# Kernel tuning notes

Hardware: AMD Instinct MI355X
Metric: run time of the kernel (lower is better)

Reference implementation:

```python
import jax, jax.numpy as jnp
import numpy as np

N_HEADS = 16
EPS = 1e-4


def setup_inputs() -> dict:
    key = jax.random.key(0)
    ks = jax.random.split(key, 9)
    B, L, E = 4, 4096, 1024
    s = 1.0 / np.sqrt(E)
    return {
        "x": jax.random.normal(ks[0], (B, L, E), dtype=jnp.float32),
        "Wq": jax.random.normal(ks[1], (E, E), dtype=jnp.float32) * s,
        "bq": jax.random.normal(ks[2], (E,), dtype=jnp.float32) * 0.01,
        "Wk": jax.random.normal(ks[3], (E, E), dtype=jnp.float32) * s,
        "bk": jax.random.normal(ks[4], (E,), dtype=jnp.float32) * 0.01,
        "Wv": jax.random.normal(ks[5], (E, E), dtype=jnp.float32) * s,
        "bv": jax.random.normal(ks[6], (E,), dtype=jnp.float32) * 0.01,
        "Wo": jax.random.normal(ks[7], (E, E), dtype=jnp.float32) * s,
        "bo": jax.random.normal(ks[8], (E,), dtype=jnp.float32) * 0.01,
    }


def _cosformer(x, Wq, bq, Wk, bk, Wv, bv, Wo, bo):
    B, L, E = x.shape
    H = N_HEADS
    hd = E // H
    # torch Linear: y = x @ W.T + b; self-attention so q=k=v source is x
    q = jax.nn.relu(jnp.einsum('ble,fe->blf', x, Wq) + bq)
    k = jax.nn.relu(jnp.einsum('ble,fe->blf', x, Wk) + bk)
    v = jnp.einsum('ble,fe->blf', x, Wv) + bv
    # (B, L, E) -> (B*H, L, hd)  [matches torch view(L, B*H, hd).transpose(0,1)]
    def split_heads(t):
        return t.reshape(B, L, H, hd).transpose(0, 2, 1, 3).reshape(B * H, L, hd)
    q, k, v = split_heads(q), split_heads(k), split_heads(v)
    m = L  # src_len == tgt_len
    idx = (np.pi / 2) * jnp.arange(1, m + 1, dtype=jnp.float32) / m  # (m,)
    sin = jnp.sin(idx)[None, :, None]
    cos = jnp.cos(idx)[None, :, None]
    q_ = jnp.concatenate([q * sin, q * cos], axis=-1)  # (BH, L, 2hd)
    k_ = jnp.concatenate([k * sin, k * cos], axis=-1)
    kv = jnp.einsum('nld,nlm->ndm', k_, v)             # (BH, 2hd, hd)
    z = 1.0 / jnp.maximum(jnp.einsum('nld,nd->nl', q_, k_.sum(axis=1)), EPS)
    attn = jnp.einsum('nld,ndm->nlm', q_, kv) * z[:, :, None]  # (BH, L, hd)
    # (B*H, L, hd) -> (B, L, E)
    out = attn.reshape(B, H, L, hd).transpose(0, 2, 1, 3).reshape(B, L, E)
    return jnp.einsum('ble,fe->blf', out, Wo) + bo


def reference(x, Wq, bq, Wk, bk, Wv, bv, Wo, bo):
    return _cosformer(x, Wq, bq, Wk, bk, Wv, bv, Wo, bo)
```

## Files before the change

kernel.cpp:

```cpp
#include <hip/hip_runtime.h>


typedef unsigned short u16;
typedef unsigned int u32;
typedef __attribute__((ext_vector_type(8))) __bf16 bf16x8;
typedef __attribute__((ext_vector_type(4))) float f32x4;

#define PI_HALF 1.57079632679489662f
#define EPS_Z 1e-4f

__device__ __forceinline__ u16 f32_to_bf16(float f) {
    union { float f; unsigned int u; } x; x.f = f;
    unsigned int lsb = (x.u >> 16) & 1u;
    x.u += 0x7fffu + lsb;
    return (u16)(x.u >> 16);
}

typedef __attribute__((address_space(1))) void amdgpu_global_t;
typedef __attribute__((address_space(3))) void amdgpu_lds_t;
__device__ __forceinline__ void async_load16(const u16* g, u16* l) {
    __builtin_amdgcn_global_load_lds((amdgpu_global_t*)g, (amdgpu_lds_t*)l, 16, 0, 0);
}

__global__ __launch_bounds__(256) void cvt_all(const float* __restrict__ x,
                                               const float* __restrict__ w0,
                                               const float* __restrict__ w1,
                                               const float* __restrict__ w2,
                                               const float* __restrict__ w3,
                                               u16* __restrict__ xb,
                                               u16* __restrict__ wcat) {
    const int bid = blockIdx.x;
    const float* src;
    u16* dst;
    int i;
    if (bid < 16384) {
        src = x; dst = xb;
        i = bid * 256 + threadIdx.x;
    } else {
        const int wb = bid - 16384;
        const int wsel = wb >> 10;
        src = (wsel == 0) ? w0 : (wsel == 1) ? w1 : (wsel == 2) ? w2 : w3;
        dst = wcat + (size_t)wsel * 1048576;
        i = (wb & 1023) * 256 + threadIdx.x;
    }
    float4 f = ((const float4*)src)[i];
    ushort4 o;
    o.x = f32_to_bf16(f.x); o.y = f32_to_bf16(f.y);
    o.z = f32_to_bf16(f.z); o.w = f32_to_bf16(f.w);
    ((ushort4*)dst)[i] = o;
}

__device__ __forceinline__ void gemm256_core(const u16* __restrict__ Abase,
                                             const u16* __restrict__ Bbase,
                                             u16* As, u16* Bs,
                                             f32x4 (&acc)[8][4]) {
    const int tid  = threadIdx.x;
    const int wave = tid >> 6;
    const int lane = tid & 63;
    const int quad = lane >> 4;
    const int l15  = lane & 15;
    const int wr   = wave >> 2;
    const int wc   = wave & 3;
    const int srow = tid >> 3;
    const int scg  = (tid & 7) ^ (srow & 7);

    const u16* Ag = Abase + ((long)srow << 10) + scg * 8;
    const u16* Bg = Bbase + ((long)srow << 10) + scg * 8;

    auto stage = [&](const u16* g, u16* lb, int hs, int t) {
        async_load16(g + ((long)hs << 16) + (t << 6), lb + hs * 4096);
    };
    auto rdA = [&](const u16* buf, int mf, int kk) -> bf16x8 {
        const int R = wr * 128 + mf * 16 + l15;
        return *(const bf16x8*)(buf + R * 64 + ((kk * 32 + quad * 8) ^ ((R & 7) * 8)));
    };
    auto rdB = [&](const u16* buf, int nf, int kk) -> bf16x8 {
        const int R = wc * 64 + nf * 16 + l15;
        return *(const bf16x8*)(buf + R * 64 + ((kk * 32 + quad * 8) ^ ((R & 7) * 8)));
    };

    bf16x8 a[4][2], b[4][2];
    auto mfma8 = [&](int i0, int j0) {
        __builtin_amdgcn_s_setprio(1);
#pragma unroll
        for (int i = 0; i < 4; ++i)
#pragma unroll
            for (int j = 0; j < 2; ++j)
#pragma unroll
                for (int kk = 0; kk < 2; ++kk)
                    acc[i0 + i][j0 + j] = __builtin_amdgcn_mfma_f32_16x16x32_bf16(
                        a[i][kk], b[j0 + j][kk], acc[i0 + i][j0 + j], 0, 0, 0);
        __builtin_amdgcn_s_setprio(0);
    };

#pragma unroll
    for (int hs = 0; hs < 4; ++hs) stage(Ag, As + wave * 512, hs, 0);
#pragma unroll
    for (int hs = 0; hs < 4; ++hs) stage(Bg, Bs + wave * 512, hs, 0);
#pragma unroll
    for (int hs = 0; hs < 4; ++hs) stage(Ag, As + 16384 + wave * 512, hs, 1);
#pragma unroll
    for (int hs = 0; hs < 4; ++hs) stage(Bg, Bs + 16384 + wave * 512, hs, 1);
    asm volatile("s_waitcnt vmcnt(8)" ::: "memory");
    __builtin_amdgcn_s_barrier();

#pragma unroll 1
    for (int t = 0; t < 16; ++t) {
        const int cur = t & 1;
        const u16* Ab = As + cur * 16384;
        const u16* Bb = Bs + cur * 16384;
        u16* lA = As + cur * 16384 + wave * 512;
        u16* lB = Bs + cur * 16384 + wave * 512;
        const bool pf = (t < 14);

#pragma unroll
        for (int i = 0; i < 4; ++i) { a[i][0] = rdA(Ab, i, 0); a[i][1] = rdA(Ab, i, 1); }
#pragma unroll
        for (int j = 0; j < 2; ++j) { b[j][0] = rdB(Bb, j, 0); b[j][1] = rdB(Bb, j, 1); }
        mfma8(0, 0);
#pragma unroll
        for (int j = 2; j < 4; ++j) { b[j][0] = rdB(Bb, j, 0); b[j][1] = rdB(Bb, j, 1); }
        mfma8(0, 2);
#pragma unroll
        for (int i = 0; i < 4; ++i) { a[i][0] = rdA(Ab, i + 4, 0); a[i][1] = rdA(Ab, i + 4, 1); }
        mfma8(4, 0);

        __builtin_amdgcn_s_barrier();
        asm volatile("" ::: "memory");
        if (pf) {
#pragma unroll
            for (int hs = 0; hs < 4; ++hs) stage(Bg, lB, hs, t + 2);
#pragma unroll
            for (int hs = 0; hs < 4; ++hs) stage(Ag, lA, hs, t + 2);
        }
        mfma8(4, 2);
        if (pf) {
            asm volatile("s_waitcnt vmcnt(8)" ::: "memory");
        } else {
            asm volatile("s_waitcnt vmcnt(0)" ::: "memory");
        }
        __builtin_amdgcn_s_barrier();
        asm volatile("" ::: "memory");
    }
}

__global__ __launch_bounds__(512, 2) void gemm_qkv(const u16* __restrict__ A,
                                                   const u16* __restrict__ Wcat,
                                                   const float* __restrict__ bq,
                                                   const float* __restrict__ bk,
                                                   const float* __restrict__ bv,
                                                   u16* __restrict__ qo,
                                                   u16* __restrict__ ko,
                                                   u16* __restrict__ vo) {
    __shared__ __align__(16) u16 As[32768];
    __shared__ __align__(16) u16 Bs[32768];
    const int bid = blockIdx.x;
    const int swz = (bid & 7) * 96 + (bid >> 3);
    const int bx  = swz / 12;
    const int byy = swz - bx * 12;
    const long tileM = (long)bx * 256;

    f32x4 acc[8][4] = {};
    gemm256_core(A + (tileM << 10), Wcat + ((long)byy << 18), As, Bs, acc);

    const int tid  = (int)threadIdx.x;
    const int wave = tid >> 6;
    const int lane = tid & 63;
    const int quad = lane >> 4, l15 = lane & 15;
    const int wr = wave >> 2, wc = wave & 3;
    const int mat = byy >> 2;
    const float* bias = (mat == 0) ? bq : (mat == 1) ? bk : bv;
    u16* outp = (mat == 0) ? qo : (mat == 1) ? ko : vo;
    const bool relu = (mat < 2);
    const int ncol0 = (byy & 3) * 256;

    const int rloc = tid >> 5;
    const int c8   = (tid & 31) * 8;
#pragma unroll 1
    for (int pass = 0; pass < 2; ++pass) {
        __syncthreads();
        if (wr == pass) {
#pragma unroll
            for (int i = 0; i < 8; ++i)
#pragma unroll
                for (int j = 0; j < 4; ++j) {
                    const int col = wc * 64 + j * 16 + l15;
                    const float bb = bias[ncol0 + col];
#pragma unroll
                    for (int r = 0; r < 4; ++r) {
                        const int row = i * 16 + quad * 4 + r;
                        float v = acc[i][j][r] + bb;
                        if (relu) v = fmaxf(v, 0.0f);
                        As[row * 256 + col] = f32_to_bf16(v);
                    }
                }
        }
        __syncthreads();
        const long gr0 = tileM + pass * 128;
#pragma unroll
        for (int it = 0; it < 8; ++it) {
            const int row = it * 16 + rloc;
            uint4 t4 = *(const uint4*)&As[row * 256 + c8];
            *(uint4*)&outp[(gr0 + row) * 1024 + ncol0 + c8] = t4;
        }
    }
}

__global__ __launch_bounds__(512, 2) void gemm_o(const u16* __restrict__ A,
                                                 const u16* __restrict__ Bw,
                                                 const float* __restrict__ bias,
                                                 float* __restrict__ Cout) {
    __shared__ __align__(16) u16 As[32768];
    __shared__ __align__(16) u16 Bs[32768];
    const int bid = blockIdx.x;
    const int swz = (bid & 7) * 32 + (bid >> 3);
    const long tileM = (long)(swz >> 2) * 256;
    const long tileN = (long)(swz & 3) * 256;

    f32x4 acc[8][4] = {};
    gemm256_core(A + (tileM << 10), Bw + (tileN << 10), As, Bs, acc);

    const int wave = (int)threadIdx.x >> 6;
    const int lane = (int)threadIdx.x & 63;
    const int quad = lane >> 4, l15 = lane & 15;
    const int wr = wave >> 2, wc = wave & 3;
#pragma unroll
    for (int j = 0; j < 4; ++j) {
        const long n = tileN + wc * 64 + j * 16 + l15;
        const float bb = bias[n];
#pragma unroll
        for (int i = 0; i < 8; ++i) {
            const long m0 = tileM + wr * 128 + i * 16 + quad * 4;
#pragma unroll
            for (int r = 0; r < 4; ++r)
                Cout[(m0 + r) * 1024 + n] = acc[i][j][r] + bb;
        }
    }
}

__global__ __launch_bounds__(256) void kv_mfma(const u16* __restrict__ kmat,
                                               const u16* __restrict__ vmat,
                                               float* __restrict__ part) {
    __shared__ u16 Ak[64 * 72];
    __shared__ u16 Bv[64 * 72];
    const int tid = threadIdx.x;
    const int wave = tid >> 6, lane = tid & 63;
    const int quad = lane >> 4, l15 = lane & 15;
    const int head = blockIdx.y;
    const int b = head >> 4, h = head & 15;
    const int l0 = blockIdx.x * 512;
    const int sl = tid >> 3;
    const int sc8 = tid & 7;
    const int scol = sl ^ ((sc8 & 3) << 3);
    const int krow_base = (wave & 1) * 32;
    const bool use_cos = (wave >> 1) != 0;
    const int mbase = wave * 32;

    float sv[8], cv[8], s2[8], c2[8];
#pragma unroll
    for (int e = 0; e < 8; e++) {
        float ang = (PI_HALF / 4096.0f) * (float)(l0 + quad * 8 + e + 1);
        sv[e] = sinf(ang); cv[e] = cosf(ang);
        float ang2 = ang + (PI_HALF / 4096.0f) * 32.0f;
        s2[e] = sinf(ang2); c2[e] = cosf(ang2);
    }
    const float cD = 0.99969881869620422f;
    const float sD = 0.02454122852291229f;

    bf16x8 onesf;
#pragma unroll
    for (int e = 0; e < 8; e++)
        onesf[e] = (l15 == 0) ? (__bf16)1.0f : (__bf16)0.0f;

    f32x4 acc[2][5] = {};

    long row = ((long)b * 4096 + l0 + sl) * 1024 + h * 64 + sc8 * 8;
    uint4 kkA = *(const uint4*)(kmat + row);
    uint4 vvA = *(const uint4*)(vmat + row);
    uint4 kkB = *(const uint4*)(kmat + row + 32 * 1024);
    uint4 vvB = *(const uint4*)(vmat + row + 32 * 1024);

#pragma unroll 1
    for (int kt = 0; kt < 8; kt++) {
        uint4 kkA_n = {}, vvA_n = {}, kkB_n = {}, vvB_n = {};
        if (kt < 7) {
            row += 64 * 1024;
            kkA_n = *(const uint4*)(kmat + row);
            vvA_n = *(const uint4*)(vmat + row);
            kkB_n = *(const uint4*)(kmat + row + 32 * 1024);
            vvB_n = *(const uint4*)(vmat + row + 32 * 1024);
        }
        {
            const u16* kp = (const u16*)&kkA;
            const u16* vp = (const u16*)&vvA;
            const u16* kp2 = (const u16*)&kkB;
            const u16* vp2 = (const u16*)&vvB;
#pragma unroll
            for (int e = 0; e < 8; e++) {
                const int d = sc8 * 8 + e;
                Ak[d * 72 + scol]      = kp[e];
                Bv[d * 72 + scol]      = vp[e];
                Ak[d * 72 + scol + 32] = kp2[e];
                Bv[d * 72 + scol + 32] = vp2[e];
            }
        }
        __syncthreads();

        bf16x8 af[2][2];
#pragma unroll
        for (int i = 0; i < 2; i++) {
            const int d = krow_base + i * 16 + l15;
            const int q2 = (quad ^ ((d >> 3) & 3)) * 8;
#pragma unroll
            for (int kk = 0; kk < 2; kk++) {
                bf16x8 raw = *(const bf16x8*)&Ak[d * 72 + kk * 32 + q2];
                bf16x8 sc;
#pragma unroll
                for (int e = 0; e < 8; e++) {
                    const float s = use_cos ? (kk ? c2[e] : cv[e])
                                            : (kk ? s2[e] : sv[e]);
                    sc[e] = (__bf16)((float)raw[e] * s);
                }
                af[i][kk] = sc;
            }
        }
        bf16x8 bfr[5][2];
#pragma unroll
        for (int j = 0; j < 4; j++) {
            const int n = j * 16 + l15;
            const int q2 = (quad ^ ((n >> 3) & 3)) * 8;
            bfr[j][0] = *(const bf16x8*)&Bv[n * 72 + q2];
            bfr[j][1] = *(const bf16x8*)&Bv[n * 72 + 32 + q2];
        }
        bfr[4][0] = onesf; bfr[4][1] = onesf;
#pragma unroll
        for (int i = 0; i < 2; i++)
#pragma unroll
            for (int j = 0; j < 5; j++) {
                acc[i][j] = __builtin_amdgcn_mfma_f32_16x16x32_bf16(
                    af[i][0], bfr[j][0], acc[i][j], 0, 0, 0);
                acc[i][j] = __builtin_amdgcn_mfma_f32_16x16x32_bf16(
                    af[i][1], bfr[j][1], acc[i][j], 0, 0, 0);
            }

#pragma unroll
        for (int e = 0; e < 8; e++) {
            float ns = sv[e] * cD + cv[e] * sD;
            cv[e] = cv[e] * cD - sv[e] * sD;
            sv[e] = ns;
            ns = s2[e] * cD + c2[e] * sD;
            c2[e] = c2[e] * cD - s2[e] * sD;
            s2[e] = ns;
        }
        __syncthreads();
        kkA = kkA_n; vvA = vvA_n; kkB = kkB_n; vvB = vvB_n;
    }

    float* op = part + ((long)blockIdx.x * 64 + head) * 10240;
#pragma unroll
    for (int i = 0; i < 2; i++)
#pragma unroll
        for (int j = 0; j < 5; j++)
#pragma unroll
            for (int r = 0; r < 4; r++)
                op[(mbase + i * 16 + quad * 4 + r) * 80 + j * 16 + l15] = acc[i][j][r];
}

__global__ __launch_bounds__(256) void kv_reduce_t(const float* __restrict__ part,
                                                   u16* __restrict__ Bt) {
    __shared__ float accs[32 * 81];
    const int head = blockIdx.y, d2t = blockIdx.x;
    const float* bp = part + (long)head * 10240 + d2t * 32 * 80;
    for (int idx = threadIdx.x; idx < 2560; idx += 256) {
        float s = 0.0f;
#pragma unroll
        for (int c = 0; c < 8; c++) s += bp[(long)c * 655360 + idx];
        const int d2 = idx / 80, n = idx - d2 * 80;
        accs[d2 * 81 + n] = s;
    }
    __syncthreads();
    for (int idx = threadIdx.x; idx < 2560; idx += 256) {
        const int n = idx >> 5, d2 = idx & 31;
        Bt[(long)head * 10240 + n * 128 + d2t * 32 + d2] = f32_to_bf16(accs[d2 * 81 + n]);
    }
}

__global__ __launch_bounds__(256) void attn_mfma(const u16* __restrict__ qb,
                                                 const u16* __restrict__ Bt,
                                                 u16* __restrict__ merged) {
    __shared__ __align__(16) u16 As[128 * 72];
    __shared__ __align__(16) u16 Bs[80 * 136];
    const int tid = threadIdx.x;
    const int wave = tid >> 6, lane = tid & 63;
    const int quad = lane >> 4, l15 = lane & 15;
    const int head = blockIdx.y;
    const int b = head >> 4, h = head & 15;
    const int tm0 = blockIdx.x * 256;
    const long b4 = (long)b * 4096;
    const int wm = wave * 32;

    for (int c = tid; c < 1280; c += 256) {
        const int row = c >> 4, c16 = c & 15;
        uint4 t = *(const uint4*)(Bt + (long)head * 10240 + row * 128 + c16 * 8);
        *(uint4*)&Bs[row * 136 + c16 * 8] = t;
    }

#pragma unroll 1
    for (int half = 0; half < 2; ++half) {
        const int tm = tm0 + half * 128;
        __syncthreads();
        for (int c = tid; c < 1024; c += 256) {
            const int row = c >> 3, c8 = c & 7;
            uint4 t = *(const uint4*)(qb + (b4 + tm + row) * 1024 + h * 64 + c8 * 8);
            *(uint4*)&As[row * 72 + c8 * 8] = t;
        }
        float snl[2], csl[2];
#pragma unroll
        for (int i = 0; i < 2; i++) {
            const int l = tm + wm + i * 16 + l15;
            const float idx = PI_HALF * (float)(l + 1) * (1.0f / 4096.0f);
            snl[i] = sinf(idx); csl[i] = cosf(idx);
        }
        __syncthreads();

        f32x4 acc[2][5] = {};
#pragma unroll
        for (int kb = 0; kb < 4; kb++) {
            const int qc = (kb & 1) * 32 + quad * 8;
            bf16x8 af[2];
#pragma unroll
            for (int i = 0; i < 2; i++) {
                bf16x8 raw = *(const bf16x8*)&As[(wm + i * 16 + l15) * 72 + qc];
                const float s = (kb < 2) ? snl[i] : csl[i];
                bf16x8 sc;
#pragma unroll
                for (int e = 0; e < 8; e++) sc[e] = (__bf16)((float)raw[e] * s);
                af[i] = sc;
            }
            bf16x8 bf[5];
#pragma unroll
            for (int j = 0; j < 5; j++)
                bf[j] = *(const bf16x8*)&Bs[(j * 16 + l15) * 136 + kb * 32 + quad * 8];
#pragma unroll
            for (int i = 0; i < 2; i++)
#pragma unroll
                for (int j = 0; j < 5; j++)
                    acc[i][j] = __builtin_amdgcn_mfma_f32_16x16x32_bf16(
                        af[i], bf[j], acc[i][j], 0, 0, 0);
        }

        __syncthreads();
#pragma unroll
        for (int i = 0; i < 2; i++) {
            float z[4];
#pragma unroll
            for (int r = 0; r < 4; r++) {
                const float den = __shfl(acc[i][4][r], lane & 0x30, 64);
                z[r] = 1.0f / fmaxf(den, EPS_Z);
            }
#pragma unroll
            for (int j = 0; j < 4; j++)
#pragma unroll
                for (int r = 0; r < 4; r++) {
                    const int row = wm + i * 16 + quad * 4 + r;
                    As[row * 64 + j * 16 + l15] = f32_to_bf16(acc[i][j][r] * z[r]);
                }
        }
        __syncthreads();
        const int rloc = tid >> 3, c8o = (tid & 7) * 8;
#pragma unroll
        for (int it = 0; it < 4; ++it) {
            const int row = it * 32 + rloc;
            uint4 t4 = *(const uint4*)&As[row * 64 + c8o];
            *(uint4*)&merged[(b4 + tm + row) * 1024 + h * 64 + c8o] = t4;
        }
    }
}

extern "C" void kernel_launch(void* const* d_in, const int* in_sizes, int n_in,
                              void* d_out, int out_size, void* d_ws, size_t ws_size,
                              hipStream_t stream) {
    (void)in_sizes; (void)n_in; (void)out_size; (void)ws_size;
    const float* x  = (const float*)d_in[0];
    const float* Wq = (const float*)d_in[1];
    const float* bq = (const float*)d_in[2];
    const float* Wk = (const float*)d_in[3];
    const float* bk = (const float*)d_in[4];
    const float* Wv = (const float*)d_in[5];
    const float* bv = (const float*)d_in[6];
    const float* Wo = (const float*)d_in[7];
    const float* bo = (const float*)d_in[8];
    float* out = (float*)d_out;

    const int E = 1024;
    char* ws = (char*)d_ws;
    const size_t MB = 1048576;
    u16* xb   = (u16*)(ws);
    u16* qb   = (u16*)(ws + 32 * MB);
    u16* kb   = (u16*)(ws + 64 * MB);
    u16* vb   = (u16*)(ws + 96 * MB);
    u16* wcat = (u16*)(ws + 128 * MB);
    u16* wob  = wcat + 3 * (size_t)E * E;
    u16* Btb  = (u16*)(ws + 136 * MB);
    float* part = (float*)xb;
    u16* mergedb = kb;

    cvt_all<<<dim3(20480), dim3(256), 0, stream>>>(x, Wq, Wk, Wv, Wo, xb, wcat);

    gemm_qkv<<<dim3(768), dim3(512), 0, stream>>>(xb, wcat, bq, bk, bv, qb, kb, vb);

    kv_mfma<<<dim3(8, 64), dim3(256), 0, stream>>>(kb, vb, part);
    kv_reduce_t<<<dim3(4, 64), dim3(256), 0, stream>>>(part, Btb);
    attn_mfma<<<dim3(16, 64), dim3(256), 0, stream>>>(qb, Btb, mergedb);

    gemm_o<<<dim3(256), dim3(512), 0, stream>>>(mergedb, wob, bo, out);
}
```

Baseline: 341.1 us.

## Fuse fp32-to-bf16 conversion of x into QKV GEMM A-tile loading

Drops the separate pass that converts the 64 MB fp32 activation x to bf16. The QKV GEMM now loads fp32 A tiles into registers, converts them with packed bf16 conversion instructions and writes them to LDS, while B still uses async global-to-LDS loads. This removes a full read and write of x, but each GEMM tile reads fp32 A twice over (once per 12 column tiles) and the A staging path now goes through registers, which raises register pressure and the risk of pipeline stalls.

```diff
diff --git a/kernel.cpp b/kernel.cpp
--- a/kernel.cpp
+++ b/kernel.cpp
@@ -15,6 +15,11 @@
     x.u += 0x7fffu + lsb;
     return (u16)(x.u >> 16);
 }
+__device__ __forceinline__ u32 cvt_pk2(float a, float b) {
+    u32 r;
+    asm("v_cvt_pk_bf16_f32 %0, %1, %2" : "=v"(r) : "v"(a), "v"(b));
+    return r;
+}
 
 typedef __attribute__((address_space(1))) void amdgpu_global_t;
 typedef __attribute__((address_space(3))) void amdgpu_lds_t;
@@ -22,27 +27,15 @@
     __builtin_amdgcn_global_load_lds((amdgpu_global_t*)g, (amdgpu_lds_t*)l, 16, 0, 0);
 }
 
-__global__ __launch_bounds__(256) void cvt_all(const float* __restrict__ x,
-                                               const float* __restrict__ w0,
-                                               const float* __restrict__ w1,
-                                               const float* __restrict__ w2,
-                                               const float* __restrict__ w3,
-                                               u16* __restrict__ xb,
-                                               u16* __restrict__ wcat) {
-    const int bid = blockIdx.x;
-    const float* src;
-    u16* dst;
-    int i;
-    if (bid < 16384) {
-        src = x; dst = xb;
-        i = bid * 256 + threadIdx.x;
-    } else {
-        const int wb = bid - 16384;
-        const int wsel = wb >> 10;
-        src = (wsel == 0) ? w0 : (wsel == 1) ? w1 : (wsel == 2) ? w2 : w3;
-        dst = wcat + (size_t)wsel * 1048576;
-        i = (wb & 1023) * 256 + threadIdx.x;
-    }
+__global__ __launch_bounds__(256) void cvt_w4(const float* __restrict__ w0,
+                                              const float* __restrict__ w1,
+                                              const float* __restrict__ w2,
+                                              const float* __restrict__ w3,
+                                              u16* __restrict__ wcat) {
+    const float* src = (blockIdx.y == 0) ? w0 : (blockIdx.y == 1) ? w1
+                     : (blockIdx.y == 2) ? w2 : w3;
+    u16* dst = wcat + (size_t)blockIdx.y * 1048576;
+    int i = blockIdx.x * 256 + threadIdx.x;
     float4 f = ((const float4*)src)[i];
     ushort4 o;
     o.x = f32_to_bf16(f.x); o.y = f32_to_bf16(f.y);
@@ -144,7 +137,128 @@
     }
 }
 
-__global__ __launch_bounds__(512, 2) void gemm_qkv(const u16* __restrict__ A,
+__device__ __forceinline__ void gemm256_f32a(const float* __restrict__ Af,
+                                             const u16* __restrict__ Bbase,
+                                             u16* As, u16* Bs,
+                                             f32x4 (&acc)[8][4]) {
+    const int tid  = threadIdx.x;
+    const int wave = tid >> 6;
+    const int lane = tid & 63;
+    const int quad = lane >> 4;
+    const int l15  = lane & 15;
+    const int wr   = wave >> 2;
+    const int wc   = wave & 3;
+    const int srow = tid >> 3;
+    const int c8   = (tid & 7) * 8;
+    const int scg  = (tid & 7) ^ (srow & 7);
+    const int wcol = c8 ^ ((srow & 7) * 8);
+
+    const float* Ax = Af + ((long)srow << 10) + c8;
+    const u16*   Bg = Bbase + ((long)srow << 10) + scg * 8;
+
+    auto stageB = [&](u16* lb, int hs, int t) {
+        async_load16(Bg + ((long)hs << 16) + (t << 6), lb + hs * 4096);
+    };
+    auto rdA = [&](const u16* buf, int mf, int kk) -> bf16x8 {
+        const int R = wr * 128 + mf * 16 + l15;
+        return *(const bf16x8*)(buf + R * 64 + ((kk * 32 + quad * 8) ^ ((R & 7) * 8)));
+    };
+    auto rdB = [&](const u16* buf, int nf, int kk) -> bf16x8 {
+        const int R = wc * 64 + nf * 16 + l15;
+        return *(const bf16x8*)(buf + R * 64 + ((kk * 32 + quad * 8) ^ ((R & 7) * 8)));
+    };
+
+    float4 ar[8];
+    auto loadA = [&](int t) {
+#pragma unroll
+        for (int hs = 0; hs < 4; ++hs) {
+            const float* p = Ax + ((long)hs << 16) + (t << 6);
+            ar[hs * 2]     = *(const float4*)p;
+            ar[hs * 2 + 1] = *(const float4*)(p + 4);
+        }
+    };
+    auto writeA = [&](u16* base) {
+#pragma unroll
+        for (int hs = 0; hs < 4; ++hs) {
+            uint4 pk;
+            pk.x = cvt_pk2(ar[hs * 2].x,     ar[hs * 2].y);
+            pk.y = cvt_pk2(ar[hs * 2].z,     ar[hs * 2].w);
+            pk.z = cvt_pk2(ar[hs * 2 + 1].x, ar[hs * 2 + 1].y);
+            pk.w = cvt_pk2(ar[hs * 2 + 1].z, ar[hs * 2 + 1].w);
+            *(uint4*)(base + hs * 4096 + srow * 64 + wcol) = pk;
+        }
+    };
+
+    bf16x8 a[4][2], b[4][2];
+    auto mfma8 = [&](int i0, int j0) {
+        __builtin_amdgcn_s_setprio(1);
+#pragma unroll
+        for (int i = 0; i < 4; ++i)
+#pragma unroll
+            for (int j = 0; j < 2; ++j)
+#pragma unroll
+                for (int kk = 0; kk < 2; ++kk)
+                    acc[i0 + i][j0 + j] = __builtin_amdgcn_mfma_f32_16x16x32_bf16(
+                        a[i][kk], b[j0 + j][kk], acc[i0 + i][j0 + j], 0, 0, 0);
+        __builtin_amdgcn_s_setprio(0);
+    };
+
+    loadA(0);
+    writeA(As);
+    loadA(1);
+    writeA(As + 16384);
+#pragma unroll
+    for (int hs = 0; hs < 4; ++hs) stageB(Bs + wave * 512, hs, 0);
+#pragma unroll
+    for (int hs = 0; hs < 4; ++hs) stageB(Bs + 16384 + wave * 512, hs, 1);
+    loadA(2);
+    asm volatile("s_waitcnt vmcnt(8)" ::: "memory");
+    asm volatile("s_waitcnt lgkmcnt(0)" ::: "memory");
+    __builtin_amdgcn_s_barrier();
+
+#pragma unroll 1
+    for (int t = 0; t < 16; ++t) {
+        const int cur = t & 1;
+        const u16* Ab = As + cur * 16384;
+        const u16* Bb = Bs + cur * 16384;
+        u16* lB = Bs + cur * 16384 + wave * 512;
+        const bool pf = (t < 14);
+        const bool pw = (t <= 13);
+        const bool pi = (t <= 12);
+
+#pragma unroll
+        for (int i = 0; i < 4; ++i) { a[i][0] = rdA(Ab, i, 0); a[i][1] = rdA(Ab, i, 1); }
+#pragma unroll
+        for (int j = 0; j < 2; ++j) { b[j][0] = rdB(Bb, j, 0); b[j][1] = rdB(Bb, j, 1); }
+        mfma8(0, 0);
+#pragma unroll
+        for (int j = 2; j < 4; ++j) { b[j][0] = rdB(Bb, j, 0); b[j][1] = rdB(Bb, j, 1); }
+        mfma8(0, 2);
+#pragma unroll
+        for (int i = 0; i < 4; ++i) { a[i][0] = rdA(Ab, i + 4, 0); a[i][1] = rdA(Ab, i + 4, 1); }
+        mfma8(4, 0);
+
+        __builtin_amdgcn_s_barrier();
+        asm volatile("" ::: "memory");
+        if (pf) {
+#pragma unroll
+            for (int hs = 0; hs < 4; ++hs) stageB(lB, hs, t + 2);
+        }
+        mfma8(4, 2);
+        if (pw) writeA(As + cur * 16384);
+        if (pf) {
+            asm volatile("s_waitcnt vmcnt(4)" ::: "memory");
+        } else {
+            asm volatile("s_waitcnt vmcnt(0)" ::: "memory");
+        }
+        asm volatile("s_waitcnt lgkmcnt(0)" ::: "memory");
+        if (pi) loadA(t + 3);
+        __builtin_amdgcn_s_barrier();
+        asm volatile("" ::: "memory");
+    }
+}
+
+__global__ __launch_bounds__(512, 2) void gemm_qkv(const float* __restrict__ X,
                                                    const u16* __restrict__ Wcat,
                                                    const float* __restrict__ bq,
                                                    const float* __restrict__ bk,
@@ -161,7 +275,7 @@
     const long tileM = (long)bx * 256;
 
     f32x4 acc[8][4] = {};
-    gemm256_core(A + (tileM << 10), Wcat + ((long)byy << 18), As, Bs, acc);
+    gemm256_f32a(X + (tileM << 10), Wcat + ((long)byy << 18), As, Bs, acc);
 
     const int tid  = (int)threadIdx.x;
     const int wave = tid >> 6;
@@ -495,19 +609,18 @@
     const int E = 1024;
     char* ws = (char*)d_ws;
     const size_t MB = 1048576;
-    u16* xb   = (u16*)(ws);
+    float* part = (float*)(ws);
     u16* qb   = (u16*)(ws + 32 * MB);
     u16* kb   = (u16*)(ws + 64 * MB);
     u16* vb   = (u16*)(ws + 96 * MB);
     u16* wcat = (u16*)(ws + 128 * MB);
     u16* wob  = wcat + 3 * (size_t)E * E;
     u16* Btb  = (u16*)(ws + 136 * MB);
-    float* part = (float*)xb;
     u16* mergedb = kb;
 
-    cvt_all<<<dim3(20480), dim3(256), 0, stream>>>(x, Wq, Wk, Wv, Wo, xb, wcat);
-
-    gemm_qkv<<<dim3(768), dim3(512), 0, stream>>>(xb, wcat, bq, bk, bv, qb, kb, vb);
+    cvt_w4<<<dim3(1024, 4), dim3(256), 0, stream>>>(Wq, Wk, Wv, Wo, wcat);
+
+    gemm_qkv<<<dim3(768), dim3(512), 0, stream>>>(x, wcat, bq, bk, bv, qb, kb, vb);
 
     kv_mfma<<<dim3(8, 64), dim3(256), 0, stream>>>(kb, vb, part);
     kv_reduce_t<<<dim3(4, 64), dim3(256), 0, stream>>>(part, Btb);
```

Measured after the change: 377.6 us. 1.11x slower.
